# Optimization experiments

Hardware: AMD Instinct MI355X
Metric: run time of the kernel (lower is better)

Reference implementation:

```python
import jax, jax.numpy as jnp
import numpy as np

N = 400_000      # total nodes in batched graph
E = 6_400_000    # total edges (avg degree 16)
G = 6_400        # total small graphs
B = 64           # samples; num[i] graphs per sample, sum(num)=G
F = 31           # feature dim (hard-coded in TAG)
K = 2            # TAGConv hops
L = 5            # number of TAGConv layers
MAXG = 120       # max graphs per sample (120*31 pad)


def setup_inputs() -> dict:
    key = jax.random.key(0)
    ks = jax.random.split(key, 8)
    x = jax.random.normal(ks[0], (N, F), dtype=jnp.float32)
    src = jax.random.randint(ks[1], (E,), 0, N, dtype=jnp.int32)
    dst = jax.random.randint(ks[2], (E,), 0, N, dtype=jnp.int32)
    # contiguous (sorted) graph assignment, every graph non-empty (~62 nodes each)
    graph_ids = jnp.asarray((np.arange(N, dtype=np.int64) * G) // N, dtype=jnp.int32)
    num = jnp.full((B,), G // B, dtype=jnp.int32)  # 100 graphs per sample
    Ws = jax.random.normal(ks[3], (L, (K + 1) * F, F), dtype=jnp.float32) * 0.1
    bs = jax.random.normal(ks[4], (L, F), dtype=jnp.float32) * 0.01
    w_gate = jax.random.normal(ks[5], (F,), dtype=jnp.float32) * 0.1
    b_gate = jax.random.normal(ks[6], (1,), dtype=jnp.float32) * 0.01
    return {"x": x, "Ws": Ws, "bs": bs, "w_gate": w_gate, "b_gate": b_gate,
            "src": src, "dst": dst, "graph_ids": graph_ids, "num": num}


def reference(x, Ws, bs, w_gate, b_gate, src, dst, graph_ids, num):
    # symmetric normalization: norm = in_deg^{-1/2}, deg clamped to >=1 (DGL TAGConv)
    deg = jax.ops.segment_sum(jnp.ones((E,), x.dtype), dst, num_segments=N)
    norm = jnp.clip(deg, 1.0, None) ** -0.5  # [N]

    def tagconv(h, W, b):
        fstack = [h]
        cur = h
        for _ in range(K):
            cur = norm[:, None] * cur
            cur = jax.ops.segment_sum(cur[src], dst, num_segments=N)  # SPMM hop
            cur = norm[:, None] * cur
            fstack.append(cur)
        return jnp.concatenate(fstack, axis=-1) @ W + b  # [N, F]

    h = x
    for l in range(L):
        h = jax.nn.relu(tagconv(h, Ws[l], bs[l]))

    # GlobalAttentionPooling: segment softmax over gate scores, weighted sum
    gate = h @ w_gate + b_gate[0]                                   # [N]
    gmax = jax.ops.segment_max(gate, graph_ids, num_segments=G)     # [G]
    e = jnp.exp(gate - gmax[graph_ids])
    den = jax.ops.segment_sum(e, graph_ids, num_segments=G)
    alpha = e / den[graph_ids]
    rep = jax.ops.segment_sum(alpha[:, None] * h, graph_ids, num_segments=G)  # [G, F]

    # split by num, flatten, pad to 120*31, stack
    csum = jnp.cumsum(num)
    offsets = jnp.concatenate([jnp.zeros((1,), jnp.int32), csum.astype(jnp.int32)])
    g = jnp.arange(G, dtype=jnp.int32)
    sample_id = jnp.searchsorted(csum, g, side="right").astype(jnp.int32)  # [G]
    pos = g - offsets[sample_id]
    out = jnp.zeros((B, MAXG, F), rep.dtype).at[sample_id, pos].set(rep)
    return out.reshape(B, MAXG * F)
```

## Files before the change

kernel.cpp:

```cpp
#include <hip/hip_runtime.h>
#include <hip/hip_bf16.h>

#define FDIM 31
#define FPAD 32
#define RSTRIDE 16

#define CBITS 11
#define CW    (1 << CBITS)
#define MAXBUK 256
#define TILE 4096

typedef int      iv4 __attribute__((ext_vector_type(4)));
typedef unsigned uv4 __attribute__((ext_vector_type(4)));

__device__ __forceinline__ float bf_lo(unsigned u) { return __uint_as_float(u << 16); }
__device__ __forceinline__ float bf_hi(unsigned u) { return __uint_as_float(u & 0xFFFF0000u); }
__device__ __forceinline__ unsigned pack2(float lo, float hi) {
    unsigned a = __float_as_uint(lo), b = __float_as_uint(hi);
    unsigned ra = (a + 0x7FFFu + ((a >> 16) & 1u)) >> 16;
    unsigned rb = (b + 0x7FFFu + ((b >> 16) & 1u)) >> 16;
    return ra | (rb << 16);
}

__device__ __forceinline__ int lb_gid(const int* __restrict__ gid, int Ntot, int g) {
    int lo = 0, hi = Ntot;
    while (lo < hi) { int mid = (lo + hi) >> 1; if (gid[mid] < g) lo = mid + 1; else hi = mid; }
    return lo;
}

__global__ __launch_bounds__(256) void multisplit_kernel(
    const int* __restrict__ src, const int* __restrict__ dst,
    int* __restrict__ gcnt, int* __restrict__ bucketed,
    int cap, int E, int nbuk)
{
    __shared__ int ordered[TILE];
    __shared__ int hist[MAXBUK];
    __shared__ int lofs[MAXBUK + 1];
    __shared__ int base_[MAXBUK];
    __shared__ int cur[MAXBUK];
    const int tid = threadIdx.x;
    const int e0 = blockIdx.x * TILE;
    const int n = min(TILE, E - e0);
    if (tid < MAXBUK) hist[tid] = 0;
    __syncthreads();
    for (int i = tid; i < n; i += 256)
        atomicAdd(&hist[dst[e0 + i] >> CBITS], 1);
    __syncthreads();
    if (tid == 0) {
        int a = 0;
        for (int b = 0; b < nbuk; ++b) { lofs[b] = a; a += hist[b]; }
        lofs[nbuk] = a;
    }
    __syncthreads();
    if (tid < nbuk) {
        int h = hist[tid];
        base_[tid] = h ? atomicAdd(&gcnt[tid], h) : 0;
        cur[tid] = lofs[tid];
    }
    __syncthreads();
    for (int i = tid; i < n; i += 256) {
        int s = src[e0 + i], d = dst[e0 + i];
        int b = d >> CBITS;
        int r = atomicAdd(&cur[b], 1);
        ordered[r] = (s << CBITS) | (d & (CW - 1));
    }
    __syncthreads();
    for (int i = tid; i < n; i += 256) {
        int lo = 0, hi = nbuk;
        while (hi - lo > 1) {
            int mid = (lo + hi) >> 1;
            if (lofs[mid] <= i) lo = mid; else hi = mid;
        }
        int b = lo;
        int pos = base_[b] + (i - lofs[b]);
        if (pos < cap) bucketed[(size_t)b * cap + pos] = ordered[i];
    }
}

__global__ void small_scans_kernel(const int* __restrict__ num, int* __restrict__ soff, int Bn,
                                   const int* __restrict__ gcnt, int* __restrict__ bbase,
                                   int nbuk, int cap) {
    if (threadIdx.x == 0 && blockIdx.x == 0) {
        int acc = 0; soff[0] = 0;
        for (int i = 0; i < Bn; ++i) { acc += num[i]; soff[i + 1] = acc; }
        int a = 0;
        for (int b = 0; b < nbuk; ++b) {
            bbase[b] = a;
            a += ((min(gcnt[b], cap) + 7) & ~7) + 7 * CW;
        }
    }
}

__global__ __launch_bounds__(1024) void bucket_build_kernel(
    const int* __restrict__ bucketed, const int* __restrict__ gcnt,
    const int* __restrict__ bbase,
    int* __restrict__ rowbeg, int* __restrict__ rowend,
    float* __restrict__ normv, float* __restrict__ invn,
    int* __restrict__ col,
    int cap, int N, int nbuk)
{
    __shared__ int hist[CW];
    __shared__ int lcur[CW];
    const int b = blockIdx.x, tid = threadIdx.x;
    hist[tid] = 0; hist[tid + 1024] = 0;
    __syncthreads();
    const int cnt = min(gcnt[b], cap);
    const int* reg = bucketed + (size_t)b * cap;
    for (int i = tid; i < cnt; i += 1024)
        atomicAdd(&hist[reg[i] & (CW - 1)], 1);
    __syncthreads();
    int c0 = hist[tid], c1 = hist[tid + 1024];
    int p0 = (c0 + 7) & ~7, p1 = (c1 + 7) & ~7;
    __syncthreads();
    hist[tid] = p0; hist[tid + 1024] = p1;
    __syncthreads();
    for (int off = 1; off < CW; off <<= 1) {
        int a0 = (tid >= off) ? hist[tid - off] : 0;
        int a1 = (tid + 1024 >= off) ? hist[tid + 1024 - off] : 0;
        __syncthreads();
        hist[tid] += a0; hist[tid + 1024] += a1;
        __syncthreads();
    }
    const int base = bbase[b];
    const int base_node = b << CBITS;
    int r0 = -1, r1 = -1;
    int node = base_node + tid;
    if (node < N) {
        r0 = base + hist[tid] - p0;
        rowbeg[node] = r0; rowend[node] = r0 + p0; lcur[tid] = r0;
        int cr = c0 > 0 ? c0 : 1;
        normv[node] = rsqrtf((float)cr);
        invn[node]  = sqrtf((float)cr);
    }
    node = base_node + tid + 1024;
    if (node < N) {
        r1 = base + hist[tid + 1024] - p1;
        rowbeg[node] = r1; rowend[node] = r1 + p1; lcur[tid + 1024] = r1;
        int cr = c1 > 0 ? c1 : 1;
        normv[node] = rsqrtf((float)cr);
        invn[node]  = sqrtf((float)cr);
    }
    __syncthreads();
    for (int i = tid; i < cnt; i += 1024) {
        int e = reg[i];
        int p = atomicAdd(&lcur[e & (CW - 1)], 1);
        col[p] = e >> CBITS;
    }
    if (r0 >= 0) for (int j = r0 + c0; j < r0 + p0; ++j) col[j] = N;
    if (r1 >= 0) for (int j = r1 + c1; j < r1 + p1; ++j) col[j] = N;
}

__global__ void cast_x_kernel(const float* __restrict__ x, const float* __restrict__ normv,
                              unsigned* __restrict__ A, int N) {
    int idx = blockIdx.x * 256 + threadIdx.x;
    if (idx >= (N + 1) * RSTRIDE) return;
    int n = idx >> 4, q = idx & 15;
    if (n >= N) { A[idx] = 0u; return; }
    float nv = normv[n];
    int f0 = 2 * q, f1 = 2 * q + 1;
    float lo = (f0 < FDIM) ? nv * x[(size_t)n * FDIM + f0] : 0.0f;
    float hi = (f1 < FDIM) ? nv * x[(size_t)n * FDIM + f1] : 0.0f;
    A[idx] = pack2(lo, hi);
}

#define ACC_EDGE(vN)                                                   \
    acc0 += bf_lo(vN.x); acc1 += bf_hi(vN.x);                          \
    acc2 += bf_lo(vN.y); acc3 += bf_hi(vN.y);                          \
    acc4 += bf_lo(vN.z); acc5 += bf_hi(vN.z);                          \
    acc6 += bf_lo(vN.w); acc7 += bf_hi(vN.w);

__global__ __launch_bounds__(256) void spmm_kernel(const unsigned* __restrict__ Hin,
                                                   unsigned* __restrict__ Hout,
                                                   const int* __restrict__ rowbeg,
                                                   const int* __restrict__ rowend,
                                                   const int* __restrict__ col,
                                                   const float* __restrict__ normv, int N) {
    int node = blockIdx.x * 64 + (threadIdx.x >> 2);
    int sub = threadIdx.x & 3;
    if (node > N) return;
    if (node == N) {
        uv4 z = (uv4)0;
        __builtin_nontemporal_store(z, (uv4*)(Hout + (size_t)N * RSTRIDE) + sub);
        return;
    }
    int s = rowbeg[node];
    int nit = (rowend[node] - s) >> 3;
    const iv4* cl = (const iv4*)(col + s);
    float acc0 = 0.f, acc1 = 0.f, acc2 = 0.f, acc3 = 0.f;
    float acc4 = 0.f, acc5 = 0.f, acc6 = 0.f, acc7 = 0.f;
    iv4 ca = __builtin_nontemporal_load(cl);
    iv4 cb = __builtin_nontemporal_load(cl + 1);
    for (int it = 0; it < nit; ++it) {
        uint4 v0 = *((const uint4*)(Hin + (size_t)ca.x * RSTRIDE) + sub);
        uint4 v1 = *((const uint4*)(Hin + (size_t)ca.y * RSTRIDE) + sub);
        uint4 v2 = *((const uint4*)(Hin + (size_t)ca.z * RSTRIDE) + sub);
        uint4 v3 = *((const uint4*)(Hin + (size_t)ca.w * RSTRIDE) + sub);
        uint4 v4 = *((const uint4*)(Hin + (size_t)cb.x * RSTRIDE) + sub);
        uint4 v5 = *((const uint4*)(Hin + (size_t)cb.y * RSTRIDE) + sub);
        uint4 v6 = *((const uint4*)(Hin + (size_t)cb.z * RSTRIDE) + sub);
        uint4 v7 = *((const uint4*)(Hin + (size_t)cb.w * RSTRIDE) + sub);
        const iv4* nx = cl + ((it + 1 < nit) ? 2 : 0);
        iv4 na = __builtin_nontemporal_load(nx);
        iv4 nb = __builtin_nontemporal_load(nx + 1);
        cl += 2;
        ACC_EDGE(v0) ACC_EDGE(v1) ACC_EDGE(v2) ACC_EDGE(v3)
        ACC_EDGE(v4) ACC_EDGE(v5) ACC_EDGE(v6) ACC_EDGE(v7)
        ca = na; cb = nb;
    }
    float nv = normv[node];
    float nn2 = nv * nv;
    uv4 o;
    o.x = pack2(nn2 * acc0, nn2 * acc1);
    o.y = pack2(nn2 * acc2, nn2 * acc3);
    o.z = pack2(nn2 * acc4, nn2 * acc5);
    o.w = pack2(nn2 * acc6, nn2 * acc7);
    __builtin_nontemporal_store(o, (uv4*)(Hout + (size_t)node * RSTRIDE) + sub);
}

__global__ __launch_bounds__(256) void linear_relu_kernel(const unsigned* __restrict__ A,
                                                          const unsigned* __restrict__ Bh,
                                                          const unsigned* __restrict__ Ch,
                                                          const float* __restrict__ W,
                                                          const float* __restrict__ bias,
                                                          unsigned* __restrict__ out_h,
                                                          float* __restrict__ gatev,
                                                          const float* __restrict__ w_gate,
                                                          const float* __restrict__ b_gate,
                                                          const float* __restrict__ normv,
                                                          const float* __restrict__ invn,
                                                          int do_gate, int N) {
    int n = blockIdx.x * 256 + threadIdx.x;
    if (n >= N) return;
    float out[FDIM];
#pragma unroll
    for (int j = 0; j < FDIM; ++j) out[j] = 0.0f;
#pragma unroll 1
    for (int blk = 0; blk < 3; ++blk) {
        const unsigned* bp = (blk == 0) ? A : ((blk == 1) ? Bh : Ch);
        const uint4* r4p = (const uint4*)(bp + (size_t)n * RSTRIDE);
        uint4 r4[4];
#pragma unroll
        for (int q = 0; q < 4; ++q) r4[q] = r4p[q];
        const unsigned* ru = (const unsigned*)r4;
        float rr[FPAD];
#pragma unroll
        for (int q = 0; q < RSTRIDE; ++q) { rr[2 * q] = bf_lo(ru[q]); rr[2 * q + 1] = bf_hi(ru[q]); }
        const float* Wb = W + blk * FDIM * FDIM;
#pragma unroll
        for (int i = 0; i < FDIM; ++i) {
            float v = rr[i];
#pragma unroll
            for (int j = 0; j < FDIM; ++j) out[j] = fmaf(v, Wb[i * FDIM + j], out[j]);
        }
    }
    float inv = invn[n];
#pragma unroll
    for (int j = 0; j < FDIM; ++j) out[j] = fmaxf(fmaf(out[j], inv, bias[j]), 0.0f);
    float sc = do_gate ? 1.0f : normv[n];
    unsigned* o = out_h + (size_t)n * RSTRIDE;
    uint4 w0, w1, w2, w3;
    w0.x = pack2(sc * out[0], sc * out[1]);   w0.y = pack2(sc * out[2], sc * out[3]);
    w0.z = pack2(sc * out[4], sc * out[5]);   w0.w = pack2(sc * out[6], sc * out[7]);
    w1.x = pack2(sc * out[8], sc * out[9]);   w1.y = pack2(sc * out[10], sc * out[11]);
    w1.z = pack2(sc * out[12], sc * out[13]); w1.w = pack2(sc * out[14], sc * out[15]);
    w2.x = pack2(sc * out[16], sc * out[17]); w2.y = pack2(sc * out[18], sc * out[19]);
    w2.z = pack2(sc * out[20], sc * out[21]); w2.w = pack2(sc * out[22], sc * out[23]);
    w3.x = pack2(sc * out[24], sc * out[25]); w3.y = pack2(sc * out[26], sc * out[27]);
    w3.z = pack2(sc * out[28], sc * out[29]); w3.w = pack2(sc * out[30], 0.0f);
    ((uint4*)o)[0] = w0; ((uint4*)o)[1] = w1; ((uint4*)o)[2] = w2; ((uint4*)o)[3] = w3;
    if (do_gate) {
        float g = b_gate[0];
#pragma unroll
        for (int j = 0; j < FDIM; ++j) g = fmaf(out[j], w_gate[j], g);
        gatev[n] = g;
    }
}


__global__ __launch_bounds__(64) void graph_reduce_kernel(const float* __restrict__ gate,
                                                          const int* __restrict__ gid,
                                                          const int* __restrict__ soff, int Bn,
                                                          int Ntot,
                                                          float* __restrict__ gmax,
                                                          float* __restrict__ gden) {
    int g = blockIdx.x;
    if (g >= soff[Bn]) return;
    int s = lb_gid(gid, Ntot, g), e = lb_gid(gid, Ntot, g + 1);
    float m = -1e30f;
    for (int n = s + threadIdx.x; n < e; n += 64) m = fmaxf(m, gate[n]);
#pragma unroll
    for (int o = 32; o > 0; o >>= 1) m = fmaxf(m, __shfl_xor(m, o));
    float d = 0.0f;
    for (int n = s + threadIdx.x; n < e; n += 64) d += expf(gate[n] - m);
#pragma unroll
    for (int o = 32; o > 0; o >>= 1) d += __shfl_xor(d, o);
    if (threadIdx.x == 0) { gmax[g] = m; gden[g] = d; }
}

__global__ __launch_bounds__(64) void rep_scatter_kernel(const unsigned short* __restrict__ H,
                                                         const float* __restrict__ gate,
                                                         const int* __restrict__ gid,
                                                         const int* __restrict__ soff,
                                                         int MAXG, int Ntot,
                                                         const float* __restrict__ gmax,
                                                         const float* __restrict__ gden,
                                                         float* __restrict__ out) {
    int s = blockIdx.x / MAXG;
    int pos = blockIdx.x % MAXG;
    int t = threadIdx.x;
    if (t >= FDIM) return;
    int gbeg = soff[s], gend = soff[s + 1];
    float* op = out + ((size_t)s * MAXG + pos) * FDIM + t;
    if (pos >= gend - gbeg) { *op = 0.0f; return; }
    int g = gbeg + pos;
    int ns = lb_gid(gid, Ntot, g), ne = lb_gid(gid, Ntot, g + 1);
    float m = gmax[g], den = gden[g];
    float acc = 0.0f;
    for (int n = ns; n < ne; ++n) {
        float hv = __uint_as_float((unsigned)H[(size_t)n * FPAD + t] << 16);
        acc += expf(gate[n] - m) * hv;
    }
    *op = acc / den;
}


extern "C" void kernel_launch(void* const* d_in, const int* in_sizes, int n_in,
                              void* d_out, int out_size, void* d_ws, size_t ws_size,
                              hipStream_t stream) {
    const float* x      = (const float*)d_in[0];
    const float* Ws     = (const float*)d_in[1];
    const float* bs     = (const float*)d_in[2];
    const float* w_gate = (const float*)d_in[3];
    const float* b_gate = (const float*)d_in[4];
    const int* src       = (const int*)d_in[5];
    const int* dst       = (const int*)d_in[6];
    const int* graph_ids = (const int*)d_in[7];
    const int* num       = (const int*)d_in[8];
    float* out  = (float*)d_out;

    const int N  = in_sizes[7];
    const int E  = in_sizes[5];
    const int Bn = in_sizes[8];
    const int F  = in_sizes[3];
    const int L  = in_sizes[2] / F;
    const int nW = in_sizes[1];
    const int WperL = nW / L;
    const int MAXG = out_size / (Bn * F);
    const int Gmax = Bn * MAXG;

    const int nbuk = (N + CW - 1) / CW;
    const int cap  = E / nbuk + E / (8 * nbuk) + 2048;

    char* p = (char*)d_ws;
    auto alloc = [&](size_t bytes) {
        void* r = (void*)p;
        p += (bytes + 255) & ~(size_t)255;
        return r;
    };
    unsigned* HA = (unsigned*)alloc((size_t)(N + 1) * RSTRIDE * 4);
    unsigned* HB = (unsigned*)alloc((size_t)(N + 1) * RSTRIDE * 4);
    unsigned* HC = (unsigned*)alloc((size_t)(N + 1) * RSTRIDE * 4);
    int*   colw  = (int*)alloc(((size_t)E + (size_t)nbuk * (7 * CW + 16)) * 4);
    int*   bkt   = (int*)alloc((size_t)nbuk * cap * 4);
    int*   gcnt  = (int*)alloc((size_t)nbuk * 4);
    int*   bbase = (int*)alloc((size_t)nbuk * 4);
    int*   rowb  = (int*)alloc((size_t)(N + 1) * 4);
    int*   rowe  = (int*)alloc((size_t)(N + 1) * 4);
    float* normv = (float*)alloc((size_t)N * 4);
    float* invnv = (float*)alloc((size_t)N * 4);
    float* gatev = (float*)alloc((size_t)N * 4);
    float* gmax  = (float*)alloc((size_t)Gmax * 4);
    float* gden  = (float*)alloc((size_t)Gmax * 4);
    int*   soff  = (int*)alloc((size_t)(Bn + 1) * 4);

    (void)hipMemsetAsync(gcnt, 0, (size_t)nbuk * 4, stream);

    const int NT = (E + TILE - 1) / TILE;
    multisplit_kernel<<<NT, 256, 0, stream>>>(src, dst, gcnt, bkt, cap, E, nbuk);
    small_scans_kernel<<<1, 64, 0, stream>>>(num, soff, Bn, gcnt, bbase, nbuk, cap);
    bucket_build_kernel<<<nbuk, 1024, 0, stream>>>(bkt, gcnt, bbase, rowb, rowe,
                                                   normv, invnv, colw, cap, N, nbuk);

    cast_x_kernel<<<((N + 1) * RSTRIDE + 255) / 256, 256, 0, stream>>>(x, normv, HA, N);

    const int SB = (N + 1 + 63) / 64;
    const int NB = (N + 255) / 256;
    for (int l = 0; l < L; ++l) {
        spmm_kernel<<<SB, 256, 0, stream>>>(HA, HB, rowb, rowe, colw, normv, N);
        spmm_kernel<<<SB, 256, 0, stream>>>(HB, HC, rowb, rowe, colw, normv, N);
        linear_relu_kernel<<<NB, 256, 0, stream>>>(HA, HB, HC, Ws + (size_t)l * WperL,
                                                   bs + (size_t)l * F, HA,
                                                   gatev, w_gate, b_gate, normv, invnv,
                                                   (l == L - 1) ? 1 : 0, N);
    }

    graph_reduce_kernel<<<Gmax, 64, 0, stream>>>(gatev, graph_ids, soff, Bn, N, gmax, gden);
    rep_scatter_kernel<<<Gmax, 64, 0, stream>>>((const unsigned short*)HA, gatev, graph_ids,
                                                soff, MAXG, N, gmax, gden, out);
    (void)n_in; (void)ws_size;
}
```

Baseline: 1.699 ms.

## Fuse second SpMM hop with dense linear+ReLU layer via shared memory

The second propagation hop and the per-node linear+ReLU are merged into one kernel. Each block first gathers neighbour rows for 64 nodes using 4 threads per node, stages the fp32 hop-2 result in LDS, then 64 threads apply the three weight blocks and write the layer output back into HA in place. This removes the HC buffer round trip (a bf16 write and read), one kernel launch per layer, and the hop-2 rounding to bf16. In exchange, only a quarter of each block's threads do the dense matmul phase. The launch bound of 5 blocks per SM also caps register use, which may cause spills or lower overlap.

```diff
diff --git a/kernel.cpp b/kernel.cpp
--- a/kernel.cpp
+++ b/kernel.cpp
@@ -163,11 +163,25 @@
     A[idx] = pack2(lo, hi);
 }
 
+#define GATHER8(HSRC, r0, r1, r2, r3, r4, r5, r6, r7, CA, CB)                    \
+    r0 = *((const uint4*)(HSRC + (size_t)(CA).x * RSTRIDE) + sub);               \
+    r1 = *((const uint4*)(HSRC + (size_t)(CA).y * RSTRIDE) + sub);               \
+    r2 = *((const uint4*)(HSRC + (size_t)(CA).z * RSTRIDE) + sub);               \
+    r3 = *((const uint4*)(HSRC + (size_t)(CA).w * RSTRIDE) + sub);               \
+    r4 = *((const uint4*)(HSRC + (size_t)(CB).x * RSTRIDE) + sub);               \
+    r5 = *((const uint4*)(HSRC + (size_t)(CB).y * RSTRIDE) + sub);               \
+    r6 = *((const uint4*)(HSRC + (size_t)(CB).z * RSTRIDE) + sub);               \
+    r7 = *((const uint4*)(HSRC + (size_t)(CB).w * RSTRIDE) + sub);
+
 #define ACC_EDGE(vN)                                                   \
     acc0 += bf_lo(vN.x); acc1 += bf_hi(vN.x);                          \
     acc2 += bf_lo(vN.y); acc3 += bf_hi(vN.y);                          \
     acc4 += bf_lo(vN.z); acc5 += bf_hi(vN.z);                          \
     acc6 += bf_lo(vN.w); acc7 += bf_hi(vN.w);
+
+#define ACC8(r0, r1, r2, r3, r4, r5, r6, r7)                           \
+    ACC_EDGE(r0) ACC_EDGE(r1) ACC_EDGE(r2) ACC_EDGE(r3)                \
+    ACC_EDGE(r4) ACC_EDGE(r5) ACC_EDGE(r6) ACC_EDGE(r7)
 
 __global__ __launch_bounds__(256) void spmm_kernel(const unsigned* __restrict__ Hin,
                                                    unsigned* __restrict__ Hout,
@@ -185,27 +199,22 @@
     }
     int s = rowbeg[node];
     int nit = (rowend[node] - s) >> 3;
-    const iv4* cl = (const iv4*)(col + s);
     float acc0 = 0.f, acc1 = 0.f, acc2 = 0.f, acc3 = 0.f;
     float acc4 = 0.f, acc5 = 0.f, acc6 = 0.f, acc7 = 0.f;
-    iv4 ca = __builtin_nontemporal_load(cl);
-    iv4 cb = __builtin_nontemporal_load(cl + 1);
-    for (int it = 0; it < nit; ++it) {
-        uint4 v0 = *((const uint4*)(Hin + (size_t)ca.x * RSTRIDE) + sub);
-        uint4 v1 = *((const uint4*)(Hin + (size_t)ca.y * RSTRIDE) + sub);
-        uint4 v2 = *((const uint4*)(Hin + (size_t)ca.z * RSTRIDE) + sub);
-        uint4 v3 = *((const uint4*)(Hin + (size_t)ca.w * RSTRIDE) + sub);
-        uint4 v4 = *((const uint4*)(Hin + (size_t)cb.x * RSTRIDE) + sub);
-        uint4 v5 = *((const uint4*)(Hin + (size_t)cb.y * RSTRIDE) + sub);
-        uint4 v6 = *((const uint4*)(Hin + (size_t)cb.z * RSTRIDE) + sub);
-        uint4 v7 = *((const uint4*)(Hin + (size_t)cb.w * RSTRIDE) + sub);
-        const iv4* nx = cl + ((it + 1 < nit) ? 2 : 0);
-        iv4 na = __builtin_nontemporal_load(nx);
-        iv4 nb = __builtin_nontemporal_load(nx + 1);
-        cl += 2;
-        ACC_EDGE(v0) ACC_EDGE(v1) ACC_EDGE(v2) ACC_EDGE(v3)
-        ACC_EDGE(v4) ACC_EDGE(v5) ACC_EDGE(v6) ACC_EDGE(v7)
-        ca = na; cb = nb;
+    if (nit > 0) {
+        const iv4* cl = (const iv4*)(col + s);
+        iv4 ca = __builtin_nontemporal_load(cl);
+        iv4 cb = __builtin_nontemporal_load(cl + 1);
+        for (int it = 0; it < nit; ++it) {
+            uint4 v0, v1, v2, v3, v4, v5, v6, v7;
+            GATHER8(Hin, v0, v1, v2, v3, v4, v5, v6, v7, ca, cb)
+            const iv4* nx = cl + ((it + 1 < nit) ? 2 : 0);
+            iv4 na = __builtin_nontemporal_load(nx);
+            iv4 nb = __builtin_nontemporal_load(nx + 1);
+            cl += 2;
+            ACC8(v0, v1, v2, v3, v4, v5, v6, v7)
+            ca = na; cb = nb;
+        }
     }
     float nv = normv[node];
     float nn2 = nv * nv;
@@ -217,47 +226,93 @@
     __builtin_nontemporal_store(o, (uv4*)(Hout + (size_t)node * RSTRIDE) + sub);
 }
 
-__global__ __launch_bounds__(256) void linear_relu_kernel(const unsigned* __restrict__ A,
-                                                          const unsigned* __restrict__ Bh,
-                                                          const unsigned* __restrict__ Ch,
-                                                          const float* __restrict__ W,
-                                                          const float* __restrict__ bias,
-                                                          unsigned* __restrict__ out_h,
-                                                          float* __restrict__ gatev,
-                                                          const float* __restrict__ w_gate,
-                                                          const float* __restrict__ b_gate,
-                                                          const float* __restrict__ normv,
-                                                          const float* __restrict__ invn,
-                                                          int do_gate, int N) {
-    int n = blockIdx.x * 256 + threadIdx.x;
-    if (n >= N) return;
+__global__ __launch_bounds__(256, 5) void spmm_mlp_kernel(
+    const unsigned* __restrict__ Hb,
+    unsigned* __restrict__ Ha,
+    const int* __restrict__ rowbeg,
+    const int* __restrict__ rowend,
+    const int* __restrict__ col,
+    const float* __restrict__ normv,
+    const float* __restrict__ invn,
+    const float* __restrict__ W,
+    const float* __restrict__ bias,
+    float* __restrict__ gatev,
+    const float* __restrict__ w_gate,
+    const float* __restrict__ b_gate,
+    int do_gate, int N)
+{
+    __shared__ float hcL[64 * 33];
+    const int tid = threadIdx.x;
+    {
+        int node = blockIdx.x * 64 + (tid >> 2);
+        int sub = tid & 3;
+        if (node < N) {
+            int s = rowbeg[node];
+            int nit = (rowend[node] - s) >> 3;
+            float acc0 = 0.f, acc1 = 0.f, acc2 = 0.f, acc3 = 0.f;
+            float acc4 = 0.f, acc5 = 0.f, acc6 = 0.f, acc7 = 0.f;
+            if (nit > 0) {
+                const iv4* cl = (const iv4*)(col + s);
+                iv4 ca = __builtin_nontemporal_load(cl);
+                iv4 cb = __builtin_nontemporal_load(cl + 1);
+                for (int it = 0; it < nit; ++it) {
+                    uint4 v0, v1, v2, v3, v4, v5, v6, v7;
+                    GATHER8(Hb, v0, v1, v2, v3, v4, v5, v6, v7, ca, cb)
+                    const iv4* nx = cl + ((it + 1 < nit) ? 2 : 0);
+                    iv4 na = __builtin_nontemporal_load(nx);
+                    iv4 nb = __builtin_nontemporal_load(nx + 1);
+                    cl += 2;
+                    ACC8(v0, v1, v2, v3, v4, v5, v6, v7)
+                    ca = na; cb = nb;
+                }
+            }
+            float nv = normv[node];
+            float nn2 = nv * nv;
+            float* hp = &hcL[(tid >> 2) * 33 + sub * 8];
+            hp[0] = nn2 * acc0; hp[1] = nn2 * acc1;
+            hp[2] = nn2 * acc2; hp[3] = nn2 * acc3;
+            hp[4] = nn2 * acc4; hp[5] = nn2 * acc5;
+            hp[6] = nn2 * acc6; hp[7] = nn2 * acc7;
+        }
+    }
+    __syncthreads();
+    if (tid >= 64) return;
+    int n2 = blockIdx.x * 64 + tid;
+    if (n2 >= N) return;
     float out[FDIM];
 #pragma unroll
     for (int j = 0; j < FDIM; ++j) out[j] = 0.0f;
 #pragma unroll 1
-    for (int blk = 0; blk < 3; ++blk) {
-        const unsigned* bp = (blk == 0) ? A : ((blk == 1) ? Bh : Ch);
-        const uint4* r4p = (const uint4*)(bp + (size_t)n * RSTRIDE);
+    for (int blk = 0; blk < 2; ++blk) {
+        const unsigned* bp = blk ? Hb : Ha;
+        const uint4* r4p = (const uint4*)(bp + (size_t)n2 * RSTRIDE);
         uint4 r4[4];
 #pragma unroll
         for (int q = 0; q < 4; ++q) r4[q] = r4p[q];
         const unsigned* ru = (const unsigned*)r4;
-        float rr[FPAD];
-#pragma unroll
-        for (int q = 0; q < RSTRIDE; ++q) { rr[2 * q] = bf_lo(ru[q]); rr[2 * q + 1] = bf_hi(ru[q]); }
         const float* Wb = W + blk * FDIM * FDIM;
 #pragma unroll
         for (int i = 0; i < FDIM; ++i) {
-            float v = rr[i];
+            float v = (i & 1) ? bf_hi(ru[i >> 1]) : bf_lo(ru[i >> 1]);
 #pragma unroll
             for (int j = 0; j < FDIM; ++j) out[j] = fmaf(v, Wb[i * FDIM + j], out[j]);
         }
     }
-    float inv = invn[n];
+    {
+        const float* hp = &hcL[tid * 33];
+        const float* W2 = W + 2 * FDIM * FDIM;
+#pragma unroll
+        for (int i = 0; i < FDIM; ++i) {
+            float v = hp[i];
+#pragma unroll
+            for (int j = 0; j < FDIM; ++j) out[j] = fmaf(v, W2[i * FDIM + j], out[j]);
+        }
+    }
+    float inv = invn[n2];
 #pragma unroll
     for (int j = 0; j < FDIM; ++j) out[j] = fmaxf(fmaf(out[j], inv, bias[j]), 0.0f);
-    float sc = do_gate ? 1.0f : normv[n];
-    unsigned* o = out_h + (size_t)n * RSTRIDE;
+    float sc = do_gate ? 1.0f : normv[n2];
+    unsigned* o = Ha + (size_t)n2 * RSTRIDE;
     uint4 w0, w1, w2, w3;
     w0.x = pack2(sc * out[0], sc * out[1]);   w0.y = pack2(sc * out[2], sc * out[3]);
     w0.z = pack2(sc * out[4], sc * out[5]);   w0.w = pack2(sc * out[6], sc * out[7]);
@@ -272,7 +327,7 @@
         float g = b_gate[0];
 #pragma unroll
         for (int j = 0; j < FDIM; ++j) g = fmaf(out[j], w_gate[j], g);
-        gatev[n] = g;
+        gatev[n2] = g;
     }
 }
 
@@ -359,7 +414,6 @@
     };
     unsigned* HA = (unsigned*)alloc((size_t)(N + 1) * RSTRIDE * 4);
     unsigned* HB = (unsigned*)alloc((size_t)(N + 1) * RSTRIDE * 4);
-    unsigned* HC = (unsigned*)alloc((size_t)(N + 1) * RSTRIDE * 4);
     int*   colw  = (int*)alloc(((size_t)E + (size_t)nbuk * (7 * CW + 16)) * 4);
     int*   bkt   = (int*)alloc((size_t)nbuk * cap * 4);
     int*   gcnt  = (int*)alloc((size_t)nbuk * 4);
@@ -383,15 +437,14 @@
 
     cast_x_kernel<<<((N + 1) * RSTRIDE + 255) / 256, 256, 0, stream>>>(x, normv, HA, N);
 
-    const int SB = (N + 1 + 63) / 64;
-    const int NB = (N + 255) / 256;
+    const int SB  = (N + 1 + 63) / 64;
+    const int SB2 = (N + 63) / 64;
     for (int l = 0; l < L; ++l) {
         spmm_kernel<<<SB, 256, 0, stream>>>(HA, HB, rowb, rowe, colw, normv, N);
-        spmm_kernel<<<SB, 256, 0, stream>>>(HB, HC, rowb, rowe, colw, normv, N);
-        linear_relu_kernel<<<NB, 256, 0, stream>>>(HA, HB, HC, Ws + (size_t)l * WperL,
-                                                   bs + (size_t)l * F, HA,
-                                                   gatev, w_gate, b_gate, normv, invnv,
-                                                   (l == L - 1) ? 1 : 0, N);
+        spmm_mlp_kernel<<<SB2, 256, 0, stream>>>(HB, HA, rowb, rowe, colw, normv, invnv,
+                                                 Ws + (size_t)l * WperL, bs + (size_t)l * F,
+                                                 gatev, w_gate, b_gate,
+                                                 (l == L - 1) ? 1 : 0, N);
     }
 
     graph_reduce_kernel<<<Gmax, 64, 0, stream>>>(gatev, graph_ids, soff, Bn, N, gmax, gden);
```

After: 1.612 ms. 5.1% less time.
